# Kernel tuning notes

Measured on AMD Instinct MI355X. Metric: run time of the kernel, lower is better.

## Reference

```python
import jax, jax.numpy as jnp
import numpy as np

N_ENTITIES = 100000
N_RELATIONS = 100
EMB = 64         # entity embedding_size
REL_DIM = 64     # relation_dim
BATCH = 65536


def setup_inputs() -> dict:
    key = jax.random.key(0)
    k1, k2, k3, k4, k5, k6 = jax.random.split(key, 6)
    head = jax.random.randint(k1, (BATCH,), 0, N_ENTITIES)
    relation = jax.random.randint(k2, (BATCH,), 0, N_RELATIONS)
    tail = jax.random.randint(k3, (BATCH,), 0, N_ENTITIES)
    entity_emb = jax.random.normal(k4, (N_ENTITIES, EMB), dtype=jnp.float32)
    relation_emb = jax.random.normal(k5, (N_RELATIONS, REL_DIM), dtype=jnp.float32)
    proj_emb = jax.random.normal(k6, (N_RELATIONS, EMB * REL_DIM), dtype=jnp.float32)
    return {
        "head": head,
        "relation": relation,
        "tail": tail,
        "entity_emb": entity_emb,
        "relation_emb": relation_emb,
        "proj_emb": proj_emb,
    }


def reference(head, relation, tail, entity_emb, relation_emb, proj_emb):
    h_emb = entity_emb[head]                           # [B, E]
    t_emb = entity_emb[tail]                           # [B, E]
    r_emb = relation_emb[relation]                     # [B, R]
    proj = proj_emb[relation].reshape(-1, EMB, REL_DIM)  # [B, E, R]
    h_proj = jnp.einsum('be,ber->br', h_emb, proj)     # [B, R]
    t_proj = jnp.einsum('be,ber->br', t_emb, proj)     # [B, R]
    diff = h_proj + r_emb - t_proj
    score = jnp.sum(diff * diff, axis=1)               # [B]
    return score
```

## Files before the change

### kernel.cpp

```cpp
#include <hip/hip_runtime.h>

#define BATCH   65536
#define NREL    100
#define NBB     64
#define NTILE   16

typedef __attribute__((ext_vector_type(8))) short bf16x8;
typedef __attribute__((ext_vector_type(4))) float f32x4;

__device__ __forceinline__ unsigned short f2bf(float x) {
    unsigned u = __float_as_uint(x);
    u += 0x7fffu + ((u >> 16) & 1u);
    return (unsigned short)(u >> 16);
}

__launch_bounds__(256)
__global__ void transr_prep(const int* __restrict__ relation,
                            const int* __restrict__ head,
                            const int* __restrict__ tail,
                            const float* __restrict__ proj,
                            int* __restrict__ ws_hist,
                            int* __restrict__ ws_lpfx,
                            int4* __restrict__ ws_bucket,
                            unsigned short* __restrict__ ws_pbf) {
    const int tid = threadIdx.x, bid = blockIdx.x;

    if (bid < NBB) {
        __shared__ int hist[NREL];
        __shared__ int scan[128];

        for (int r = tid; r < NREL; r += 256) hist[r] = 0;
        __syncthreads();

        const int4 v  = ((const int4*)relation)[bid * 256 + tid];
        const int4 hv = ((const int4*)head)[bid * 256 + tid];
        const int4 tv = ((const int4*)tail)[bid * 256 + tid];
        const int vals[4] = {v.x, v.y, v.z, v.w};
        const int hs[4]   = {hv.x, hv.y, hv.z, hv.w};
        const int ts[4]   = {tv.x, tv.y, tv.z, tv.w};
        int lr[4];
        #pragma unroll
        for (int k = 0; k < 4; ++k) lr[k] = atomicAdd(&hist[vals[k]], 1);
        __syncthreads();

        if (tid < 128) scan[tid] = (tid < NREL) ? hist[tid] : 0;
        __syncthreads();
        #pragma unroll
        for (int off = 1; off < 128; off <<= 1) {
            int t = 0;
            if (tid < 128 && tid >= off) t = scan[tid - off];
            __syncthreads();
            if (tid < 128) scan[tid] += t;
            __syncthreads();
        }

        const int i0 = (bid * 256 + tid) * 4;
        #pragma unroll
        for (int k = 0; k < 4; ++k) {
            const int rel = vals[k];
            ws_bucket[bid * 1024 + (scan[rel] - hist[rel]) + lr[k]] =
                make_int4(i0 + k, hs[k], ts[k], 0);
        }
        for (int r = tid; r < NREL; r += 256) {
            ws_hist[r * NBB + bid] = hist[r];
            ws_lpfx[r * NBB + bid] = scan[r] - hist[r];
        }
    } else {
        const int rel = bid - NBB;
        const int n = tid >> 2, q = tid & 3;
        const float* Pr = proj + (size_t)rel * 4096;
        unsigned short* dst = ws_pbf + (size_t)rel * 4096;
        #pragma unroll
        for (int kh = 0; kh < 2; ++kh) {
            const int khi = q * 2 + kh;
            unsigned short u[8];
            #pragma unroll
            for (int klo = 0; klo < 8; ++klo)
                u[klo] = f2bf(Pr[(khi * 8 + klo) * 64 + n]);
            *(bf16x8*)&dst[n * 64 + ((khi ^ (n & 7)) << 3)] = *(bf16x8*)u;
        }
    }
}

__launch_bounds__(256, 4)
__global__ void transr_compute(const float* __restrict__ ent,
                               const float* __restrict__ remb,
                               const int* __restrict__ ws_hist,
                               const int* __restrict__ ws_lpfx,
                               const int4* __restrict__ ws_bucket,
                               const unsigned short* __restrict__ ws_pbf,
                               float* __restrict__ out) {
    __shared__ unsigned short Abuf[64 * 64];
    __shared__ unsigned short Bbuf[64 * 64];
    __shared__ int bidx_s[64];

    const int tid   = threadIdx.x;
    const int wid   = tid >> 6;
    const int lane  = tid & 63;
    const int rel   = blockIdx.y;
    const int start = blockIdx.x << 6;

    const int hown = ws_hist[rel * NBB + lane];
    const int lpfx = ws_lpfx[rel * NBB + lane];
    int hinc = hown;
    #pragma unroll
    for (int m = 1; m < 64; m <<= 1) {
        int t = __shfl_up(hinc, m);
        if (lane >= m) hinc += t;
    }
    const int hexc = hinc - hown;
    const int cnt  = __shfl(hinc, 63);
    if (start >= cnt) return;

    const uint4* bsrc = (const uint4*)(ws_pbf + (size_t)rel * 4096) + tid * 2;
    const uint4 bimg0 = bsrc[0];
    const uint4 bimg1 = bsrc[1];

    const float* Rr = remb + rel * 64;
    f32x4 acc[4];
    #pragma unroll
    for (int f = 0; f < 4; ++f) {
        const float rv = Rr[f * 16 + (lane & 15)];
        acc[f] = (f32x4){rv, rv, rv, rv};
    }

    {
        const int row = tid >> 2, q = tid & 3;
        const int j  = start + row;
        const int jj = (j < cnt) ? j : (cnt - 1);
        int lo = 0;
        #pragma unroll
        for (int s = 32; s; s >>= 1) {
            const int c = lo + s;
            const int v = __shfl(hexc, c & 63);
            if (c < 64 && v <= jj) lo = c;
        }
        const int4 e = ws_bucket[lo * 1024 + __shfl(lpfx, lo) + (jj - __shfl(hexc, lo))];
        if (q == 0) bidx_s[row] = e.x;
        const float4* h4 = (const float4*)(ent + (size_t)e.y * 64) + q * 4;
        const float4* t4 = (const float4*)(ent + (size_t)e.z * 64) + q * 4;
        #pragma unroll
        for (int i = 0; i < 2; ++i) {
            unsigned short u[8];
            #pragma unroll
            for (int m = 0; m < 2; ++m) {
                float4 a = h4[i * 2 + m], c = t4[i * 2 + m];
                u[m * 4 + 0] = f2bf(a.x - c.x);
                u[m * 4 + 1] = f2bf(a.y - c.y);
                u[m * 4 + 2] = f2bf(a.z - c.z);
                u[m * 4 + 3] = f2bf(a.w - c.w);
            }
            const int slice = (q * 2 + i) ^ (row & 7);
            *(bf16x8*)&Abuf[row * 64 + slice * 8] = *(bf16x8*)u;
        }
    }
    {
        uint4* dst = (uint4*)Bbuf + tid * 2;
        dst[0] = bimg0;
        dst[1] = bimg1;
    }
    __syncthreads();

    const int arow = wid * 16 + (lane & 15);
    const int g    = lane >> 4;
    #pragma unroll
    for (int s = 0; s < 2; ++s) {
        const int ks = g + s * 4;
        bf16x8 av = *(const bf16x8*)&Abuf[arow * 64 + ((ks ^ (arow & 7)) * 8)];
        #pragma unroll
        for (int f = 0; f < 4; ++f) {
            const int col = f * 16 + (lane & 15);
            bf16x8 bv = *(const bf16x8*)&Bbuf[col * 64 + ((ks ^ (col & 7)) * 8)];
            acc[f] = __builtin_amdgcn_mfma_f32_16x16x32_bf16(av, bv, acc[f], 0, 0, 0);
        }
    }

    float ps[4];
    #pragma unroll
    for (int r = 0; r < 4; ++r)
        ps[r] = acc[0][r] * acc[0][r] + acc[1][r] * acc[1][r] +
                acc[2][r] * acc[2][r] + acc[3][r] * acc[3][r];
    #pragma unroll
    for (int m = 1; m < 16; m <<= 1) {
        #pragma unroll
        for (int r = 0; r < 4; ++r) ps[r] += __shfl_xor(ps[r], m, 64);
    }
    if ((lane & 15) == 0) {
        const int rowb = wid * 16 + g * 4;
        #pragma unroll
        for (int r = 0; r < 4; ++r) {
            const int j = start + rowb + r;
            if (j < cnt) out[bidx_s[rowb + r]] = ps[r];
        }
    }
}

extern "C" void kernel_launch(void* const* d_in, const int* in_sizes, int n_in,
                              void* d_out, int out_size, void* d_ws, size_t ws_size,
                              hipStream_t stream) {
    const int*   head     = (const int*)d_in[0];
    const int*   relation = (const int*)d_in[1];
    const int*   tail     = (const int*)d_in[2];
    const float* ent      = (const float*)d_in[3];
    const float* remb     = (const float*)d_in[4];
    const float* proj     = (const float*)d_in[5];
    float*       out      = (float*)d_out;

    int*  ws_hist   = (int*)d_ws;
    int*  ws_lpfx   = (int*)d_ws + 8192;
    int4* ws_bucket = (int4*)((char*)d_ws + 65536);
    unsigned short* ws_pbf =
        (unsigned short*)((char*)d_ws + 2 * 1024 * 1024);

    transr_prep<<<NBB + NREL, 256, 0, stream>>>(relation, head, tail, proj,
                                                ws_hist, ws_lpfx, ws_bucket, ws_pbf);
    transr_compute<<<dim3(NTILE, NREL), 256, 0, stream>>>(
        ent, remb, ws_hist, ws_lpfx, ws_bucket, ws_pbf, out);
}
```

Measured before the change: 20.17 us.

## Pack bucket entries into 64-bit words and process two row tiles per block

Bucket records shrink from int4 to a packed 64-bit word (16-bit batch index plus two 17-bit entity indices), halving workspace traffic between the two kernels. Each compute block now handles up to 128 rows of a relation in two 64-row tiles, so the projection matrix is loaded into LDS once per two tiles and the grid halves. The cost is doubled A-buffer LDS per block, which may lower occupancy, and less parallelism when relations have few rows.

```diff
diff --git a/kernel.cpp b/kernel.cpp
--- a/kernel.cpp
+++ b/kernel.cpp
@@ -3,7 +3,7 @@
 #define BATCH   65536
 #define NREL    100
 #define NBB     64
-#define NTILE   16
+#define NBX     8
 
 typedef __attribute__((ext_vector_type(8))) short bf16x8;
 typedef __attribute__((ext_vector_type(4))) float f32x4;
@@ -21,7 +21,7 @@
                             const float* __restrict__ proj,
                             int* __restrict__ ws_hist,
                             int* __restrict__ ws_lpfx,
-                            int4* __restrict__ ws_bucket,
+                            unsigned long long* __restrict__ ws_bucket,
                             unsigned short* __restrict__ ws_pbf) {
     const int tid = threadIdx.x, bid = blockIdx.x;
 
@@ -58,8 +58,11 @@
         #pragma unroll
         for (int k = 0; k < 4; ++k) {
             const int rel = vals[k];
-            ws_bucket[bid * 1024 + (scan[rel] - hist[rel]) + lr[k]] =
-                make_int4(i0 + k, hs[k], ts[k], 0);
+            const unsigned long long e =
+                (unsigned long long)(unsigned)(i0 + k)
+                | ((unsigned long long)(unsigned)hs[k] << 16)
+                | ((unsigned long long)(unsigned)ts[k] << 33);
+            ws_bucket[bid * 1024 + (scan[rel] - hist[rel]) + lr[k]] = e;
         }
         for (int r = tid; r < NREL; r += 256) {
             ws_hist[r * NBB + bid] = hist[r];
@@ -87,18 +90,18 @@
                                const float* __restrict__ remb,
                                const int* __restrict__ ws_hist,
                                const int* __restrict__ ws_lpfx,
-                               const int4* __restrict__ ws_bucket,
+                               const unsigned long long* __restrict__ ws_bucket,
                                const unsigned short* __restrict__ ws_pbf,
                                float* __restrict__ out) {
-    __shared__ unsigned short Abuf[64 * 64];
+    __shared__ unsigned short Abuf[2][64 * 64];
     __shared__ unsigned short Bbuf[64 * 64];
-    __shared__ int bidx_s[64];
-
-    const int tid   = threadIdx.x;
-    const int wid   = tid >> 6;
-    const int lane  = tid & 63;
-    const int rel   = blockIdx.y;
-    const int start = blockIdx.x << 6;
+    __shared__ int bidx_s[128];
+
+    const int tid    = threadIdx.x;
+    const int wid    = tid >> 6;
+    const int lane   = tid & 63;
+    const int rel    = blockIdx.y;
+    const int start0 = blockIdx.x << 7;
 
     const int hown = ws_hist[rel * NBB + lane];
     const int lpfx = ws_lpfx[rel * NBB + lane];
@@ -110,23 +113,23 @@
     }
     const int hexc = hinc - hown;
     const int cnt  = __shfl(hinc, 63);
-    if (start >= cnt) return;
+    if (start0 >= cnt) return;
+    const bool has1 = (start0 + 64) < cnt;
 
     const uint4* bsrc = (const uint4*)(ws_pbf + (size_t)rel * 4096) + tid * 2;
     const uint4 bimg0 = bsrc[0];
     const uint4 bimg1 = bsrc[1];
 
     const float* Rr = remb + rel * 64;
-    f32x4 acc[4];
-    #pragma unroll
-    for (int f = 0; f < 4; ++f) {
-        const float rv = Rr[f * 16 + (lane & 15)];
-        acc[f] = (f32x4){rv, rv, rv, rv};
-    }
-
-    {
+    float rv[4];
+    #pragma unroll
+    for (int f = 0; f < 4; ++f) rv[f] = Rr[f * 16 + (lane & 15)];
+
+    #pragma unroll
+    for (int tt = 0; tt < 2; ++tt) {
+        if (tt == 1 && !has1) break;
         const int row = tid >> 2, q = tid & 3;
-        const int j  = start + row;
+        const int j  = start0 + tt * 64 + row;
         const int jj = (j < cnt) ? j : (cnt - 1);
         int lo = 0;
         #pragma unroll
@@ -135,10 +138,14 @@
             const int v = __shfl(hexc, c & 63);
             if (c < 64 && v <= jj) lo = c;
         }
-        const int4 e = ws_bucket[lo * 1024 + __shfl(lpfx, lo) + (jj - __shfl(hexc, lo))];
-        if (q == 0) bidx_s[row] = e.x;
-        const float4* h4 = (const float4*)(ent + (size_t)e.y * 64) + q * 4;
-        const float4* t4 = (const float4*)(ent + (size_t)e.z * 64) + q * 4;
+        const unsigned long long e =
+            ws_bucket[lo * 1024 + __shfl(lpfx, lo) + (jj - __shfl(hexc, lo))];
+        const int bx = (int)(e & 0xFFFFull);
+        const int hh = (int)((e >> 16) & 0x1FFFFull);
+        const int th = (int)((e >> 33) & 0x1FFFFull);
+        if (q == 0) bidx_s[tt * 64 + row] = bx;
+        const float4* h4 = (const float4*)(ent + (size_t)hh * 64) + q * 4;
+        const float4* t4 = (const float4*)(ent + (size_t)th * 64) + q * 4;
         #pragma unroll
         for (int i = 0; i < 2; ++i) {
             unsigned short u[8];
@@ -151,7 +158,7 @@
                 u[m * 4 + 3] = f2bf(a.w - c.w);
             }
             const int slice = (q * 2 + i) ^ (row & 7);
-            *(bf16x8*)&Abuf[row * 64 + slice * 8] = *(bf16x8*)u;
+            *(bf16x8*)&Abuf[tt][row * 64 + slice * 8] = *(bf16x8*)u;
         }
     }
     {
@@ -164,33 +171,41 @@
     const int arow = wid * 16 + (lane & 15);
     const int g    = lane >> 4;
     #pragma unroll
-    for (int s = 0; s < 2; ++s) {
-        const int ks = g + s * 4;
-        bf16x8 av = *(const bf16x8*)&Abuf[arow * 64 + ((ks ^ (arow & 7)) * 8)];
-        #pragma unroll
-        for (int f = 0; f < 4; ++f) {
-            const int col = f * 16 + (lane & 15);
-            bf16x8 bv = *(const bf16x8*)&Bbuf[col * 64 + ((ks ^ (col & 7)) * 8)];
-            acc[f] = __builtin_amdgcn_mfma_f32_16x16x32_bf16(av, bv, acc[f], 0, 0, 0);
-        }
-    }
-
-    float ps[4];
-    #pragma unroll
-    for (int r = 0; r < 4; ++r)
-        ps[r] = acc[0][r] * acc[0][r] + acc[1][r] * acc[1][r] +
-                acc[2][r] * acc[2][r] + acc[3][r] * acc[3][r];
-    #pragma unroll
-    for (int m = 1; m < 16; m <<= 1) {
-        #pragma unroll
-        for (int r = 0; r < 4; ++r) ps[r] += __shfl_xor(ps[r], m, 64);
-    }
-    if ((lane & 15) == 0) {
-        const int rowb = wid * 16 + g * 4;
-        #pragma unroll
-        for (int r = 0; r < 4; ++r) {
-            const int j = start + rowb + r;
-            if (j < cnt) out[bidx_s[rowb + r]] = ps[r];
+    for (int tt = 0; tt < 2; ++tt) {
+        if (tt == 1 && !has1) break;
+        f32x4 acc[4];
+        #pragma unroll
+        for (int f = 0; f < 4; ++f) acc[f] = (f32x4){rv[f], rv[f], rv[f], rv[f]};
+
+        #pragma unroll
+        for (int s = 0; s < 2; ++s) {
+            const int ks = g + s * 4;
+            bf16x8 av = *(const bf16x8*)&Abuf[tt][arow * 64 + ((ks ^ (arow & 7)) * 8)];
+            #pragma unroll
+            for (int f = 0; f < 4; ++f) {
+                const int col = f * 16 + (lane & 15);
+                bf16x8 bv = *(const bf16x8*)&Bbuf[col * 64 + ((ks ^ (col & 7)) * 8)];
+                acc[f] = __builtin_amdgcn_mfma_f32_16x16x32_bf16(av, bv, acc[f], 0, 0, 0);
+            }
+        }
+
+        float ps[4];
+        #pragma unroll
+        for (int r = 0; r < 4; ++r)
+            ps[r] = acc[0][r] * acc[0][r] + acc[1][r] * acc[1][r] +
+                    acc[2][r] * acc[2][r] + acc[3][r] * acc[3][r];
+        #pragma unroll
+        for (int m = 1; m < 16; m <<= 1) {
+            #pragma unroll
+            for (int r = 0; r < 4; ++r) ps[r] += __shfl_xor(ps[r], m, 64);
+        }
+        if ((lane & 15) == 0) {
+            const int rowb = wid * 16 + g * 4;
+            #pragma unroll
+            for (int r = 0; r < 4; ++r) {
+                const int j = start0 + tt * 64 + rowb + r;
+                if (j < cnt) out[bidx_s[tt * 64 + rowb + r]] = ps[r];
+            }
         }
     }
 }
@@ -206,14 +221,15 @@
     const float* proj     = (const float*)d_in[5];
     float*       out      = (float*)d_out;
 
-    int*  ws_hist   = (int*)d_ws;
-    int*  ws_lpfx   = (int*)d_ws + 8192;
-    int4* ws_bucket = (int4*)((char*)d_ws + 65536);
+    int* ws_hist = (int*)d_ws;
+    int* ws_lpfx = (int*)d_ws + 8192;
+    unsigned long long* ws_bucket =
+        (unsigned long long*)((char*)d_ws + 65536);
     unsigned short* ws_pbf =
-        (unsigned short*)((char*)d_ws + 2 * 1024 * 1024);
+        (unsigned short*)((char*)d_ws + 1024 * 1024);
 
     transr_prep<<<NBB + NREL, 256, 0, stream>>>(relation, head, tail, proj,
                                                 ws_hist, ws_lpfx, ws_bucket, ws_pbf);
-    transr_compute<<<dim3(NTILE, NREL), 256, 0, stream>>>(
+    transr_compute<<<dim3(NBX, NREL), 256, 0, stream>>>(
         ent, remb, ws_hist, ws_lpfx, ws_bucket, ws_pbf, out);
 }
```

New measurement: 22.37 us. +10.9%, slower.

## Precompute bf16 head-minus-tail rows in prep kernel, shrink bucket entries

Applied to the files above, without the earlier changes.

Adds 1024 extra prep blocks that gather head and tail entity rows, subtract them, convert to bf16 and write a dense per-sample difference buffer in batch order. The bucket now stores only the sample index, and the compute kernel reads 128 bytes of precomputed bf16 per row instead of doing two random fp32 gathers. The aim is to move the latency-bound random gathers into the prep kernel, where they run alongside the histogram and projection work with more parallelism. The cost is an extra 8 MB write and read round-trip through the workspace.

```diff
diff --git a/kernel.cpp b/kernel.cpp
--- a/kernel.cpp
+++ b/kernel.cpp
@@ -3,6 +3,7 @@
 #define BATCH   65536
 #define NREL    100
 #define NBB     64
+#define NGB     1024
 #define NTILE   16
 
 typedef __attribute__((ext_vector_type(8))) short bf16x8;
@@ -19,10 +20,12 @@
                             const int* __restrict__ head,
                             const int* __restrict__ tail,
                             const float* __restrict__ proj,
+                            const float* __restrict__ ent,
                             int* __restrict__ ws_hist,
                             int* __restrict__ ws_lpfx,
-                            int4* __restrict__ ws_bucket,
-                            unsigned short* __restrict__ ws_pbf) {
+                            int* __restrict__ ws_bucket,
+                            unsigned short* __restrict__ ws_pbf,
+                            unsigned short* __restrict__ ws_dbuf) {
     const int tid = threadIdx.x, bid = blockIdx.x;
 
     if (bid < NBB) {
@@ -32,12 +35,8 @@
         for (int r = tid; r < NREL; r += 256) hist[r] = 0;
         __syncthreads();
 
-        const int4 v  = ((const int4*)relation)[bid * 256 + tid];
-        const int4 hv = ((const int4*)head)[bid * 256 + tid];
-        const int4 tv = ((const int4*)tail)[bid * 256 + tid];
+        const int4 v = ((const int4*)relation)[bid * 256 + tid];
         const int vals[4] = {v.x, v.y, v.z, v.w};
-        const int hs[4]   = {hv.x, hv.y, hv.z, hv.w};
-        const int ts[4]   = {tv.x, tv.y, tv.z, tv.w};
         int lr[4];
         #pragma unroll
         for (int k = 0; k < 4; ++k) lr[k] = atomicAdd(&hist[vals[k]], 1);
@@ -58,14 +57,13 @@
         #pragma unroll
         for (int k = 0; k < 4; ++k) {
             const int rel = vals[k];
-            ws_bucket[bid * 1024 + (scan[rel] - hist[rel]) + lr[k]] =
-                make_int4(i0 + k, hs[k], ts[k], 0);
+            ws_bucket[bid * 1024 + (scan[rel] - hist[rel]) + lr[k]] = i0 + k;
         }
         for (int r = tid; r < NREL; r += 256) {
             ws_hist[r * NBB + bid] = hist[r];
             ws_lpfx[r * NBB + bid] = scan[r] - hist[r];
         }
-    } else {
+    } else if (bid < NBB + NREL) {
         const int rel = bid - NBB;
         const int n = tid >> 2, q = tid & 3;
         const float* Pr = proj + (size_t)rel * 4096;
@@ -79,16 +77,34 @@
                 u[klo] = f2bf(Pr[(khi * 8 + klo) * 64 + n]);
             *(bf16x8*)&dst[n * 64 + ((khi ^ (n & 7)) << 3)] = *(bf16x8*)u;
         }
+    } else {
+        const int idx = (bid - NBB - NREL) * 256 + tid;
+        const int row = idx >> 2, q = idx & 3;
+        const int h = head[row], t = tail[row];
+        const float4* h4 = (const float4*)(ent + (size_t)h * 64) + q * 4;
+        const float4* t4 = (const float4*)(ent + (size_t)t * 64) + q * 4;
+        unsigned short u[16];
+        #pragma unroll
+        for (int m = 0; m < 4; ++m) {
+            float4 a = h4[m], c = t4[m];
+            u[m * 4 + 0] = f2bf(a.x - c.x);
+            u[m * 4 + 1] = f2bf(a.y - c.y);
+            u[m * 4 + 2] = f2bf(a.z - c.z);
+            u[m * 4 + 3] = f2bf(a.w - c.w);
+        }
+        bf16x8* dst = (bf16x8*)&ws_dbuf[(size_t)row * 64 + q * 16];
+        dst[0] = *(bf16x8*)&u[0];
+        dst[1] = *(bf16x8*)&u[8];
     }
 }
 
 __launch_bounds__(256, 4)
-__global__ void transr_compute(const float* __restrict__ ent,
-                               const float* __restrict__ remb,
+__global__ void transr_compute(const float* __restrict__ remb,
                                const int* __restrict__ ws_hist,
                                const int* __restrict__ ws_lpfx,
-                               const int4* __restrict__ ws_bucket,
+                               const int* __restrict__ ws_bucket,
                                const unsigned short* __restrict__ ws_pbf,
+                               const unsigned short* __restrict__ ws_dbuf,
                                float* __restrict__ out) {
     __shared__ unsigned short Abuf[64 * 64];
     __shared__ unsigned short Bbuf[64 * 64];
@@ -135,24 +151,13 @@
             const int v = __shfl(hexc, c & 63);
             if (c < 64 && v <= jj) lo = c;
         }
-        const int4 e = ws_bucket[lo * 1024 + __shfl(lpfx, lo) + (jj - __shfl(hexc, lo))];
-        if (q == 0) bidx_s[row] = e.x;
-        const float4* h4 = (const float4*)(ent + (size_t)e.y * 64) + q * 4;
-        const float4* t4 = (const float4*)(ent + (size_t)e.z * 64) + q * 4;
-        #pragma unroll
-        for (int i = 0; i < 2; ++i) {
-            unsigned short u[8];
-            #pragma unroll
-            for (int m = 0; m < 2; ++m) {
-                float4 a = h4[i * 2 + m], c = t4[i * 2 + m];
-                u[m * 4 + 0] = f2bf(a.x - c.x);
-                u[m * 4 + 1] = f2bf(a.y - c.y);
-                u[m * 4 + 2] = f2bf(a.z - c.z);
-                u[m * 4 + 3] = f2bf(a.w - c.w);
-            }
-            const int slice = (q * 2 + i) ^ (row & 7);
-            *(bf16x8*)&Abuf[row * 64 + slice * 8] = *(bf16x8*)u;
-        }
+        const int b = ws_bucket[lo * 1024 + __shfl(lpfx, lo) + (jj - __shfl(hexc, lo))];
+        if (q == 0) bidx_s[row] = b;
+        const bf16x8* src = (const bf16x8*)&ws_dbuf[(size_t)b * 64 + q * 16];
+        const bf16x8 u0 = src[0];
+        const bf16x8 u1 = src[1];
+        *(bf16x8*)&Abuf[row * 64 + (((q * 2)     ^ (row & 7)) * 8)] = u0;
+        *(bf16x8*)&Abuf[row * 64 + (((q * 2 + 1) ^ (row & 7)) * 8)] = u1;
     }
     {
         uint4* dst = (uint4*)Bbuf + tid * 2;
@@ -206,14 +211,17 @@
     const float* proj     = (const float*)d_in[5];
     float*       out      = (float*)d_out;
 
-    int*  ws_hist   = (int*)d_ws;
-    int*  ws_lpfx   = (int*)d_ws + 8192;
-    int4* ws_bucket = (int4*)((char*)d_ws + 65536);
+    int* ws_hist = (int*)d_ws;
+    int* ws_lpfx = (int*)d_ws + 8192;
+    int* ws_bucket = (int*)((char*)d_ws + 65536);
     unsigned short* ws_pbf =
+        (unsigned short*)((char*)d_ws + 512 * 1024);
+    unsigned short* ws_dbuf =
         (unsigned short*)((char*)d_ws + 2 * 1024 * 1024);
 
-    transr_prep<<<NBB + NREL, 256, 0, stream>>>(relation, head, tail, proj,
-                                                ws_hist, ws_lpfx, ws_bucket, ws_pbf);
+    transr_prep<<<NBB + NREL + NGB, 256, 0, stream>>>(
+        relation, head, tail, proj, ent,
+        ws_hist, ws_lpfx, ws_bucket, ws_pbf, ws_dbuf);
     transr_compute<<<dim3(NTILE, NREL), 256, 0, stream>>>(
-        ent, remb, ws_hist, ws_lpfx, ws_bucket, ws_pbf, out);
-}
+        remb, ws_hist, ws_lpfx, ws_bucket, ws_pbf, ws_dbuf, out);
+}
```

Result: faster. 19.50 us, median of 2 (-3.3%).
